# Performance work log

Measured on AMD Instinct MI355X. Metric: run time of the kernel, lower is better.

The kernel has to match this reference:

```python
import jax, jax.numpy as jnp
import numpy as np

T, N, D, H = 512, 64, 1024, 1024  # time, batch(envs), input dim, hidden dim


def setup_inputs() -> dict:
    key = jax.random.key(0)
    ks = jax.random.split(key, 7)
    x = jax.random.normal(ks[0], (T, N, D), jnp.float32)
    hx = jax.random.normal(ks[1], (N, H), jnp.float32)
    mask = (jax.random.uniform(ks[2], (T, N)) > 0.05).astype(jnp.float32)
    s = float(1.0 / np.sqrt(H))
    w_ih = jax.random.uniform(ks[3], (3 * H, D), jnp.float32, -s, s)
    w_hh = jax.random.uniform(ks[4], (3 * H, H), jnp.float32, -s, s)
    b_ih = jax.random.uniform(ks[5], (3 * H,), jnp.float32, -s, s)
    b_hh = jax.random.uniform(ks[6], (3 * H,), jnp.float32, -s, s)
    return {"x": x, "hx": hx, "mask": mask, "w_ih": w_ih, "w_hh": w_hh,
            "b_ih": b_ih, "b_hh": b_hh}


def reference(x, hx, mask, w_ih, w_hh, b_ih, b_hh):
    """Masked GRU scan, equivalent to the segment-splitting torch loop:
    h is multiplied by mask[t] before every step (mask==1 inside episodes,
    0 at episode boundaries, so this matches masking only at segment starts).
    """
    # Precompute input projections for all timesteps in one big GEMM: [T,N,3H]
    gi = jnp.einsum('tnd,gd->tng', x, w_ih) + b_ih

    def step(h, inp):
        gi_t, m_t = inp                       # [N,3H], [N]
        h = h * m_t[:, None]                  # reset hidden at episode starts
        gh = h @ w_hh.T + b_hh                # [N,3H]
        i_r, i_z, i_n = jnp.split(gi_t, 3, axis=-1)
        h_r, h_z, h_n = jnp.split(gh, 3, axis=-1)
        r = jax.nn.sigmoid(i_r + h_r)
        z = jax.nn.sigmoid(i_z + h_z)
        n = jnp.tanh(i_n + r * h_n)
        h_new = (1.0 - z) * n + z * h
        return h_new, h_new

    h_final, out = jax.lax.scan(step, hx, (gi, mask))
    return out, h_final
```

## Files before the change

### kernel.cpp

```cpp
#include <hip/hip_runtime.h>

#define TT 512
#define NN 64
#define DD 1024
#define HH 1024

typedef __attribute__((ext_vector_type(8))) short bf16x8;
typedef __attribute__((ext_vector_type(4))) float f32x4;
typedef __attribute__((ext_vector_type(8))) unsigned short u16x8;
typedef __attribute__((ext_vector_type(4))) int i32x4;

__device__ unsigned short g_wih[192u * 2048 * 8];
__device__ unsigned short g_whh[192u * 2048 * 8];
__device__ unsigned short g_x[2048u * 2048 * 8];
__device__ unsigned short g_gi[(size_t)2048 * 64 * 768];
__device__ unsigned g_hbuf32[2u * 4 * 16384];

__device__ __forceinline__ unsigned short f2bf(float f) {
  unsigned u = __float_as_uint(f);
  u += 0x7fffu + ((u >> 16) & 1u);
  return (unsigned short)(u >> 16);
}

__global__ void prep_kernel(const float* __restrict__ x,
                            const float* __restrict__ wih,
                            const float* __restrict__ whh) {
  const int gsz = gridDim.x * blockDim.x;
  const int gid = blockIdx.x * blockDim.x + threadIdx.x;
  for (int z = gid; z < 2 * 4 * 16384; z += gsz) g_hbuf32[z] = 0u;

  const int W8 = 192 * 2048;
  const int X8 = 2048 * 2048;
  for (int idx = gid; idx < 2 * W8 + X8; idx += gsz) {
    if (idx < 2 * W8) {
      const float* src = (idx < W8) ? wih : whh;
      unsigned short* dst = (idx < W8) ? g_wih : g_whh;
      int i8 = (idx < W8) ? idx : idx - W8;
      size_t g = (size_t)i8 * 8;
      int col = (int)(g >> 10);
      int k = (int)(g & 1023);
      int kk = k >> 5, lg = (k >> 3) & 3;
      int cg = col >> 4;
      int l = (col & 15) | (lg << 4);
      size_t o8 = ((size_t)cg * 32 + kk) * 64 + l;
      const float* p = src + g;
      float4 v0 = *(const float4*)(p);
      float4 v1 = *(const float4*)(p + 4);
      u16x8 u;
      u[0] = f2bf(v0.x); u[1] = f2bf(v0.y); u[2] = f2bf(v0.z); u[3] = f2bf(v0.w);
      u[4] = f2bf(v1.x); u[5] = f2bf(v1.y); u[6] = f2bf(v1.z); u[7] = f2bf(v1.w);
      *(u16x8*)(dst + o8 * 8) = u;
    } else {
      int i8 = idx - 2 * W8;
      size_t g = (size_t)i8 * 8;
      int row = (int)(g >> 10);
      int k = (int)(g & 1023);
      int t = row >> 6, env = row & 63;
      int eg = env >> 4;
      int kk = k >> 5, lg = (k >> 3) & 3;
      int l = (env & 15) | (lg << 4);
      size_t o8 = (((size_t)t * 4 + eg) * 32 + kk) * 64 + l;
      const float* p = x + g;
      float4 v0 = *(const float4*)(p);
      float4 v1 = *(const float4*)(p + 4);
      u16x8 u;
      u[0] = f2bf(v0.x); u[1] = f2bf(v0.y); u[2] = f2bf(v0.z); u[3] = f2bf(v0.w);
      u[4] = f2bf(v1.x); u[5] = f2bf(v1.y); u[6] = f2bf(v1.z); u[7] = f2bf(v1.w);
      *(u16x8*)(g_x + o8 * 8) = u;
    }
  }
}

__global__ __launch_bounds__(256) void gemm_gi() {
  extern __shared__ char smem[];
  unsigned short* As = (unsigned short*)smem;
  unsigned short* Bs = As + 2048 * 8;
  const int tid = threadIdx.x;
  const int bid = blockIdx.x;
  const int mblk = bid & 255, nblk = bid >> 8;
  const int w = tid >> 6, l = tid & 63;
  const int wm = w >> 1, wn = w & 1;

  u16x8 pa[8], pb[8];
  #pragma unroll
  for (int i = 0; i < 8; ++i) {
    int e = tid + i * 256;
    int mt = e >> 8, kkl = (e >> 6) & 3, lane = e & 63;
    pa[i] = *((const u16x8*)g_x  + ((size_t)(mblk * 8 + mt) * 32 + kkl) * 64 + lane);
    pb[i] = *((const u16x8*)g_wih + ((size_t)(nblk * 8 + mt) * 32 + kkl) * 64 + lane);
  }
  f32x4 acc[4][4] = {};
  for (int c = 0; c < 8; ++c) {
    __syncthreads();
    #pragma unroll
    for (int i = 0; i < 8; ++i) {
      int e = tid + i * 256;
      ((u16x8*)As)[e] = pa[i];
      ((u16x8*)Bs)[e] = pb[i];
    }
    __syncthreads();
    if (c < 7) {
      #pragma unroll
      for (int i = 0; i < 8; ++i) {
        int e = tid + i * 256;
        int mt = e >> 8, kkl = (e >> 6) & 3, lane = e & 63;
        pa[i] = *((const u16x8*)g_x  + ((size_t)(mblk * 8 + mt) * 32 + (c + 1) * 4 + kkl) * 64 + lane);
        pb[i] = *((const u16x8*)g_wih + ((size_t)(nblk * 8 + mt) * 32 + (c + 1) * 4 + kkl) * 64 + lane);
      }
    }
    #pragma unroll
    for (int kkl = 0; kkl < 4; ++kkl) {
      bf16x8 af[4], bfr[4];
      #pragma unroll
      for (int ai = 0; ai < 4; ++ai) af[ai]  = ((const bf16x8*)As)[((wm * 4 + ai) * 4 + kkl) * 64 + l];
      #pragma unroll
      for (int bi = 0; bi < 4; ++bi) bfr[bi] = ((const bf16x8*)Bs)[((wn * 4 + bi) * 4 + kkl) * 64 + l];
      #pragma unroll
      for (int ai = 0; ai < 4; ++ai)
        #pragma unroll
        for (int bi = 0; bi < 4; ++bi)
          acc[ai][bi] = __builtin_amdgcn_mfma_f32_16x16x32_bf16(af[ai], bfr[bi], acc[ai][bi], 0, 0, 0);
    }
  }
  const int jj = l & 15;
  #pragma unroll
  for (int ai = 0; ai < 4; ++ai)
    #pragma unroll
    for (int bi = 0; bi < 4; ++bi) {
      int mt = mblk * 8 + wm * 4 + ai;
      int nt = nblk * 8 + wn * 4 + bi;
      int gate = nt >> 6, jg = nt & 63;
      size_t base = ((size_t)mt * 64 + jg) * 768 + (size_t)gate * 256;
      #pragma unroll
      for (int i = 0; i < 4; ++i) {
        int env = (l >> 4) * 4 + i;
        g_gi[base + env * 16 + jj] = f2bf(acc[ai][bi][i]);
      }
    }
}

__global__ __launch_bounds__(256) void scan_kernel(const float* __restrict__ hx,
                                                   const float* __restrict__ mask,
                                                   const float* __restrict__ bih,
                                                   const float* __restrict__ bhh,
                                                   float* __restrict__ out) {
  extern __shared__ char smem[];
  unsigned short* whhL = (unsigned short*)smem;
  unsigned short* hA   = whhL + 3 * 2048 * 8;
  float* Cl = (float*)(hA + 2048 * 8);

  const int tid = threadIdx.x;
  const int bid = blockIdx.x;
  const int eg = bid >> 6, jg = bid & 63;
  const int e0 = eg * 16;
  const int w3 = tid >> 6, l = tid & 63;
  const int e_ = tid >> 4, jj = tid & 15;
  const int j = jg * 16 + jj;

  #pragma unroll 4
  for (int i = 0; i < 24; ++i) {
    int e = tid + i * 256;
    int gate = e >> 11, rem = e & 2047;
    ((u16x8*)whhL)[e] = *((const u16x8*)g_whh + (size_t)(gate * 64 + jg) * 2048 + rem);
  }

  const int kf = jg * 16 + jj;
  const int widx = (((kf >> 5) * 64) + (e_ | (((kf >> 3) & 3) << 4))) * 8 + (kf & 7);

  float hreg;
  {
    float h0 = hx[(size_t)(e0 + e_) * HH + j] * mask[e0 + e_];
    hreg = h0;
    unsigned tw = (1u << 16) | (unsigned)f2bf(h0);
    unsigned* dst = g_hbuf32 + ((size_t)eg << 14) + widx;
    asm volatile("global_store_dword %0, %1, off sc0 sc1" :: "v"(dst), "v"(tw) : "memory");
  }

  const float br  = bih[j] + bhh[j];
  const float bz  = bih[HH + j] + bhh[HH + j];
  const float bin = bih[2 * HH + j];
  const float bhn = bhh[2 * HH + j];

  unsigned short pgr, pgz, pgn;
  {
    size_t gb = ((size_t)eg * 64 + jg) * 768;
    pgr = g_gi[gb + tid]; pgz = g_gi[gb + 256 + tid]; pgn = g_gi[gb + 512 + tid];
  }

  const unsigned voff = (unsigned)tid * 32;

  for (int t = 0; t < TT; ++t) {
    int tm = (t + 1 < TT) ? (t + 1) : (TT - 1);
    float mnext = mask[tm * NN + e0 + e_];

    const unsigned* hb = g_hbuf32 + (((size_t)(t & 1) * 4 + eg) << 14);
    const unsigned tagp = (unsigned)(t + 1) << 16;
    i32x4 hv[16];
    while (true) {
      #pragma unroll
      for (int i = 0; i < 8; ++i) {
        asm volatile("global_load_dwordx4 %0, %2, %3 sc0 sc1\n\t"
                     "global_load_dwordx4 %1, %2, %3 offset:16 sc0 sc1"
                     : "=&v"(hv[2 * i]), "=&v"(hv[2 * i + 1])
                     : "v"(voff), "s"(hb + i * 2048));
      }
      asm volatile("s_waitcnt vmcnt(0)" ::: "memory");
      __builtin_amdgcn_sched_barrier(0);
      unsigned bad = 0;
      #pragma unroll
      for (int i = 0; i < 16; ++i) {
        bad |= ((unsigned)hv[i][0] ^ tagp); bad |= ((unsigned)hv[i][1] ^ tagp);
        bad |= ((unsigned)hv[i][2] ^ tagp); bad |= ((unsigned)hv[i][3] ^ tagp);
      }
      bad &= 0xFFFF0000u;
      if (__all(bad == 0)) break;
      __builtin_amdgcn_s_sleep(1);
    }

    #pragma unroll
    for (int i = 0; i < 8; ++i) {
      i32x4 a = hv[2 * i], b = hv[2 * i + 1];
      i32x4 pk;
      pk[0] = (int)__builtin_amdgcn_perm((unsigned)a[1], (unsigned)a[0], 0x05040100u);
      pk[1] = (int)__builtin_amdgcn_perm((unsigned)a[3], (unsigned)a[2], 0x05040100u);
      pk[2] = (int)__builtin_amdgcn_perm((unsigned)b[1], (unsigned)b[0], 0x05040100u);
      pk[3] = (int)__builtin_amdgcn_perm((unsigned)b[3], (unsigned)b[2], 0x05040100u);
      ((i32x4*)hA)[tid + i * 256] = pk;
    }
    __syncthreads();

    float gr  = __uint_as_float((unsigned)pgr << 16);
    float gz  = __uint_as_float((unsigned)pgz << 16);
    float gn_ = __uint_as_float((unsigned)pgn << 16);
    if (t + 1 < TT) {
      size_t gb = ((size_t)((t + 1) * 4 + eg) * 64 + jg) * 768;
      pgr = g_gi[gb + tid]; pgz = g_gi[gb + 256 + tid]; pgn = g_gi[gb + 512 + tid];
    }

    if (w3 < 3) {
      const bf16x8* ap = (const bf16x8*)hA;
      const bf16x8* bp = (const bf16x8*)whhL + (size_t)w3 * 2048;
      f32x4 acc0 = {0.f, 0.f, 0.f, 0.f}, acc1 = {0.f, 0.f, 0.f, 0.f};
      #pragma unroll 8
      for (int kk = 0; kk < 16; ++kk) {
        acc0 = __builtin_amdgcn_mfma_f32_16x16x32_bf16(ap[kk * 64 + l], bp[kk * 64 + l], acc0, 0, 0, 0);
        acc1 = __builtin_amdgcn_mfma_f32_16x16x32_bf16(ap[(kk + 16) * 64 + l], bp[(kk + 16) * 64 + l], acc1, 0, 0, 0);
      }
      int col = l & 15, r0 = (l >> 4) * 4;
      #pragma unroll
      for (int i = 0; i < 4; ++i) Cl[w3 * 256 + (r0 + i) * 16 + col] = acc0[i] + acc1[i];
    }
    __syncthreads();

    {
      float pr = gr + Cl[tid] + br;
      float pz = gz + Cl[256 + tid] + bz;
      float r = 1.f / (1.f + __expf(-pr));
      float z = 1.f / (1.f + __expf(-pz));
      float hn = Cl[512 + tid] + bhn;
      float gn = gn_ + bin + r * hn;
      float e2g = __expf(2.f * gn);
      float n = 1.f - 2.f / (e2g + 1.f);
      float hnew = (1.f - z) * n + z * hreg;
      if (t + 1 < TT) {
        float hm = hnew * mnext;
        hreg = hm;
        unsigned tw = ((unsigned)(t + 2) << 16) | (unsigned)f2bf(hm);
        unsigned* dst = g_hbuf32 + (((size_t)((t + 1) & 1) * 4 + eg) << 14) + widx;
        asm volatile("global_store_dword %0, %1, off sc0 sc1" :: "v"(dst), "v"(tw) : "memory");
      }
      out[(size_t)t * NN * HH + (size_t)(e0 + e_) * HH + j] = hnew;
      if (t == TT - 1)
        out[(size_t)TT * NN * HH + (size_t)(e0 + e_) * HH + j] = hnew;
    }
  }
}

extern "C" void kernel_launch(void* const* d_in, const int* in_sizes, int n_in,
                              void* d_out, int out_size, void* d_ws, size_t ws_size,
                              hipStream_t stream) {
  (void)in_sizes; (void)n_in; (void)d_ws; (void)ws_size; (void)out_size;
  const float* x    = (const float*)d_in[0];
  const float* hx   = (const float*)d_in[1];
  const float* mask = (const float*)d_in[2];
  const float* wih  = (const float*)d_in[3];
  const float* whh  = (const float*)d_in[4];
  const float* bih  = (const float*)d_in[5];
  const float* bhh  = (const float*)d_in[6];
  float* out = (float*)d_out;

  hipFuncSetAttribute((const void*)gemm_gi, hipFuncAttributeMaxDynamicSharedMemorySize, 65536);
  hipFuncSetAttribute((const void*)scan_kernel, hipFuncAttributeMaxDynamicSharedMemorySize, 134144);

  prep_kernel<<<2048, 256, 0, stream>>>(x, wih, whh);
  gemm_gi<<<6144, 256, 65536, stream>>>();
  scan_kernel<<<256, 256, 134144, stream>>>(hx, mask, bih, bhh, out);
}
```

Before: 2.304 ms.

## Replace tagged-value polling with per-block flags and bf16 hidden buffer

Drops the scheme where every hidden value carries a 16-bit timestep tag that all waves poll. Hidden state is now stored as plain bf16, and each producer block publishes one flag after a store drain and a block barrier. Consumers spin on 64 flags, then read half as many bytes without any repacking. The MFMA reduction is also split across four independent accumulators to shorten the dependency chain. The cost is an extra vmcnt wait plus a __syncthreads before each flag store, and ordering correctness now relies on sc0/sc1 visibility between the data and the flag.

```diff
diff --git a/kernel.cpp b/kernel.cpp
--- a/kernel.cpp
+++ b/kernel.cpp
@@ -14,7 +14,8 @@
 __device__ unsigned short g_whh[192u * 2048 * 8];
 __device__ unsigned short g_x[2048u * 2048 * 8];
 __device__ unsigned short g_gi[(size_t)2048 * 64 * 768];
-__device__ unsigned g_hbuf32[2u * 4 * 16384];
+__device__ unsigned short g_hbuf[2u * 4 * 16384];
+__device__ int g_flags[256];
 
 __device__ __forceinline__ unsigned short f2bf(float f) {
   unsigned u = __float_as_uint(f);
@@ -27,7 +28,7 @@
                             const float* __restrict__ whh) {
   const int gsz = gridDim.x * blockDim.x;
   const int gid = blockIdx.x * blockDim.x + threadIdx.x;
-  for (int z = gid; z < 2 * 4 * 16384; z += gsz) g_hbuf32[z] = 0u;
+  if (gid < 256) g_flags[gid] = 0;
 
   const int W8 = 192 * 2048;
   const int X8 = 2048 * 2048;
@@ -171,9 +172,16 @@
   {
     float h0 = hx[(size_t)(e0 + e_) * HH + j] * mask[e0 + e_];
     hreg = h0;
-    unsigned tw = (1u << 16) | (unsigned)f2bf(h0);
-    unsigned* dst = g_hbuf32 + ((size_t)eg << 14) + widx;
-    asm volatile("global_store_dword %0, %1, off sc0 sc1" :: "v"(dst), "v"(tw) : "memory");
+    unsigned short* dst = g_hbuf + ((size_t)eg << 14) + widx;
+    unsigned hw = (unsigned)f2bf(h0);
+    asm volatile("global_store_short %0, %1, off sc0 sc1" :: "v"(dst), "v"(hw) : "memory");
+  }
+  asm volatile("s_waitcnt vmcnt(0)" ::: "memory");
+  __syncthreads();
+  if (tid == 0) {
+    int* fdst = g_flags + eg * 64 + jg;
+    int one = 1;
+    asm volatile("global_store_dword %0, %1, off sc0 sc1" :: "v"(fdst), "v"(one) : "memory");
   }
 
   const float br  = bih[j] + bhh[j];
@@ -187,46 +195,34 @@
     pgr = g_gi[gb + tid]; pgz = g_gi[gb + 256 + tid]; pgn = g_gi[gb + 512 + tid];
   }
 
-  const unsigned voff = (unsigned)tid * 32;
+  const unsigned voff = (unsigned)tid * 16;
+  const int* fp = g_flags + eg * 64 + l;
 
   for (int t = 0; t < TT; ++t) {
     int tm = (t + 1 < TT) ? (t + 1) : (TT - 1);
     float mnext = mask[tm * NN + e0 + e_];
 
-    const unsigned* hb = g_hbuf32 + (((size_t)(t & 1) * 4 + eg) << 14);
-    const unsigned tagp = (unsigned)(t + 1) << 16;
-    i32x4 hv[16];
+    const int target = t + 1;
     while (true) {
-      #pragma unroll
-      for (int i = 0; i < 8; ++i) {
-        asm volatile("global_load_dwordx4 %0, %2, %3 sc0 sc1\n\t"
-                     "global_load_dwordx4 %1, %2, %3 offset:16 sc0 sc1"
-                     : "=&v"(hv[2 * i]), "=&v"(hv[2 * i + 1])
-                     : "v"(voff), "s"(hb + i * 2048));
-      }
-      asm volatile("s_waitcnt vmcnt(0)" ::: "memory");
-      __builtin_amdgcn_sched_barrier(0);
-      unsigned bad = 0;
-      #pragma unroll
-      for (int i = 0; i < 16; ++i) {
-        bad |= ((unsigned)hv[i][0] ^ tagp); bad |= ((unsigned)hv[i][1] ^ tagp);
-        bad |= ((unsigned)hv[i][2] ^ tagp); bad |= ((unsigned)hv[i][3] ^ tagp);
-      }
-      bad &= 0xFFFF0000u;
-      if (__all(bad == 0)) break;
-      __builtin_amdgcn_s_sleep(1);
-    }
-
+      int v;
+      asm volatile("global_load_dword %0, %1, off sc0 sc1\n\t"
+                   "s_waitcnt vmcnt(0)"
+                   : "=v"(v) : "v"(fp) : "memory");
+      if (__all(v >= target)) break;
+    }
+    __builtin_amdgcn_sched_barrier(0);
+
+    const unsigned* hb = (const unsigned*)g_hbuf + (((size_t)(t & 1) * 4 + eg) << 13);
+    i32x4 hv[8];
     #pragma unroll
     for (int i = 0; i < 8; ++i) {
-      i32x4 a = hv[2 * i], b = hv[2 * i + 1];
-      i32x4 pk;
-      pk[0] = (int)__builtin_amdgcn_perm((unsigned)a[1], (unsigned)a[0], 0x05040100u);
-      pk[1] = (int)__builtin_amdgcn_perm((unsigned)a[3], (unsigned)a[2], 0x05040100u);
-      pk[2] = (int)__builtin_amdgcn_perm((unsigned)b[1], (unsigned)b[0], 0x05040100u);
-      pk[3] = (int)__builtin_amdgcn_perm((unsigned)b[3], (unsigned)b[2], 0x05040100u);
-      ((i32x4*)hA)[tid + i * 256] = pk;
-    }
+      asm volatile("global_load_dwordx4 %0, %1, %2 sc0 sc1"
+                   : "=v"(hv[i]) : "v"(voff), "s"(hb + i * 1024));
+    }
+    asm volatile("s_waitcnt vmcnt(0)" ::: "memory");
+    __builtin_amdgcn_sched_barrier(0);
+    #pragma unroll
+    for (int i = 0; i < 8; ++i) ((i32x4*)hA)[tid + i * 256] = hv[i];
     __syncthreads();
 
     float gr  = __uint_as_float((unsigned)pgr << 16);
@@ -240,15 +236,21 @@
     if (w3 < 3) {
       const bf16x8* ap = (const bf16x8*)hA;
       const bf16x8* bp = (const bf16x8*)whhL + (size_t)w3 * 2048;
-      f32x4 acc0 = {0.f, 0.f, 0.f, 0.f}, acc1 = {0.f, 0.f, 0.f, 0.f};
+      f32x4 a0 = {0.f,0.f,0.f,0.f}, a1 = {0.f,0.f,0.f,0.f};
+      f32x4 a2 = {0.f,0.f,0.f,0.f}, a3 = {0.f,0.f,0.f,0.f};
       #pragma unroll 8
-      for (int kk = 0; kk < 16; ++kk) {
-        acc0 = __builtin_amdgcn_mfma_f32_16x16x32_bf16(ap[kk * 64 + l], bp[kk * 64 + l], acc0, 0, 0, 0);
-        acc1 = __builtin_amdgcn_mfma_f32_16x16x32_bf16(ap[(kk + 16) * 64 + l], bp[(kk + 16) * 64 + l], acc1, 0, 0, 0);
+      for (int kk = 0; kk < 8; ++kk) {
+        a0 = __builtin_amdgcn_mfma_f32_16x16x32_bf16(ap[kk * 64 + l],        bp[kk * 64 + l],        a0, 0, 0, 0);
+        a1 = __builtin_amdgcn_mfma_f32_16x16x32_bf16(ap[(kk + 8) * 64 + l],  bp[(kk + 8) * 64 + l],  a1, 0, 0, 0);
+        a2 = __builtin_amdgcn_mfma_f32_16x16x32_bf16(ap[(kk + 16) * 64 + l], bp[(kk + 16) * 64 + l], a2, 0, 0, 0);
+        a3 = __builtin_amdgcn_mfma_f32_16x16x32_bf16(ap[(kk + 24) * 64 + l], bp[(kk + 24) * 64 + l], a3, 0, 0, 0);
       }
+      f32x4 s01, s23, s;
+      #pragma unroll
+      for (int i = 0; i < 4; ++i) { s01[i] = a0[i] + a1[i]; s23[i] = a2[i] + a3[i]; s[i] = s01[i] + s23[i]; }
       int col = l & 15, r0 = (l >> 4) * 4;
       #pragma unroll
-      for (int i = 0; i < 4; ++i) Cl[w3 * 256 + (r0 + i) * 16 + col] = acc0[i] + acc1[i];
+      for (int i = 0; i < 4; ++i) Cl[w3 * 256 + (r0 + i) * 16 + col] = s[i];
     }
     __syncthreads();
 
@@ -262,13 +264,22 @@
       float e2g = __expf(2.f * gn);
       float n = 1.f - 2.f / (e2g + 1.f);
       float hnew = (1.f - z) * n + z * hreg;
+
       if (t + 1 < TT) {
         float hm = hnew * mnext;
         hreg = hm;
-        unsigned tw = ((unsigned)(t + 2) << 16) | (unsigned)f2bf(hm);
-        unsigned* dst = g_hbuf32 + (((size_t)((t + 1) & 1) * 4 + eg) << 14) + widx;
-        asm volatile("global_store_dword %0, %1, off sc0 sc1" :: "v"(dst), "v"(tw) : "memory");
+        unsigned short* dst = g_hbuf + (((size_t)((t + 1) & 1) * 4 + eg) << 14) + widx;
+        unsigned hw = (unsigned)f2bf(hm);
+        asm volatile("global_store_short %0, %1, off sc0 sc1" :: "v"(dst), "v"(hw) : "memory");
+        asm volatile("s_waitcnt vmcnt(0)" ::: "memory");
+        __syncthreads();
+        if (tid == 0) {
+          int* fdst = g_flags + eg * 64 + jg;
+          int fv = t + 2;
+          asm volatile("global_store_dword %0, %1, off sc0 sc1" :: "v"(fdst), "v"(fv) : "memory");
+        }
       }
+
       out[(size_t)t * NN * HH + (size_t)(e0 + e_) * HH + j] = hnew;
       if (t == TT - 1)
         out[(size_t)TT * NN * HH + (size_t)(e0 + e_) * HH + j] = hnew;
```

Measured after the change: 2.886 ms. +25.2%, slower.

## Poll hidden-state exchange per chunk with 64-slot ring and remapped blocks

Applied to the files above, without the earlier changes.

Enlarges the tagged hidden-state exchange buffer from a double buffer to a 64-slot ring and remaps block ids so blocks sharing an env group are spread differently. The first read now uses plain loads, and only the stale chunks are re-polled with coherent loads, with ready chunks packed into LDS as they arrive. The h@W_hh MFMA loop is split into four independent accumulators, and the mask load is moved after the poll. The aim is to cut cross-block spin latency and MFMA dependency stalls. The risk is that the first non-coherent read may see cached stale data, forcing a retry pass, and the larger buffer costs more zero-initialisation in prep.

```diff
diff --git a/kernel.cpp b/kernel.cpp
--- a/kernel.cpp
+++ b/kernel.cpp
@@ -9,12 +9,13 @@
 typedef __attribute__((ext_vector_type(4))) float f32x4;
 typedef __attribute__((ext_vector_type(8))) unsigned short u16x8;
 typedef __attribute__((ext_vector_type(4))) int i32x4;
+typedef __attribute__((ext_vector_type(2))) int i32x2;
 
 __device__ unsigned short g_wih[192u * 2048 * 8];
 __device__ unsigned short g_whh[192u * 2048 * 8];
 __device__ unsigned short g_x[2048u * 2048 * 8];
 __device__ unsigned short g_gi[(size_t)2048 * 64 * 768];
-__device__ unsigned g_hbuf32[2u * 4 * 16384];
+__device__ unsigned g_hbuf32[64u * 4 * 16384];
 
 __device__ __forceinline__ unsigned short f2bf(float f) {
   unsigned u = __float_as_uint(f);
@@ -27,7 +28,7 @@
                             const float* __restrict__ whh) {
   const int gsz = gridDim.x * blockDim.x;
   const int gid = blockIdx.x * blockDim.x + threadIdx.x;
-  for (int z = gid; z < 2 * 4 * 16384; z += gsz) g_hbuf32[z] = 0u;
+  for (int z = gid; z < 64 * 4 * 16384; z += gsz) g_hbuf32[z] = 0u;
 
   const int W8 = 192 * 2048;
   const int X8 = 2048 * 2048;
@@ -151,7 +152,8 @@
 
   const int tid = threadIdx.x;
   const int bid = blockIdx.x;
-  const int eg = bid >> 6, jg = bid & 63;
+  const int eg = (bid & 7) >> 1;
+  const int jg = ((bid >> 3) << 1) | (bid & 1);
   const int e0 = eg * 16;
   const int w3 = tid >> 6, l = tid & 63;
   const int e_ = tid >> 4, jj = tid & 15;
@@ -187,45 +189,48 @@
     pgr = g_gi[gb + tid]; pgz = g_gi[gb + 256 + tid]; pgn = g_gi[gb + 512 + tid];
   }
 
-  const unsigned voff = (unsigned)tid * 32;
+  const unsigned voff = (unsigned)tid * 16;
 
   for (int t = 0; t < TT; ++t) {
-    int tm = (t + 1 < TT) ? (t + 1) : (TT - 1);
-    float mnext = mask[tm * NN + e0 + e_];
-
-    const unsigned* hb = g_hbuf32 + (((size_t)(t & 1) * 4 + eg) << 14);
+    const unsigned* hb = g_hbuf32 + ((((size_t)(t & 63)) * 4 + eg) << 14);
     const unsigned tagp = (unsigned)(t + 1) << 16;
+    const i32x4* hp = (const i32x4*)hb + tid;
     i32x4 hv[16];
-    while (true) {
-      #pragma unroll
-      for (int i = 0; i < 8; ++i) {
-        asm volatile("global_load_dwordx4 %0, %2, %3 sc0 sc1\n\t"
-                     "global_load_dwordx4 %1, %2, %3 offset:16 sc0 sc1"
-                     : "=&v"(hv[2 * i]), "=&v"(hv[2 * i + 1])
-                     : "v"(voff), "s"(hb + i * 2048));
+    #pragma unroll
+    for (int c = 0; c < 16; ++c) hv[c] = hp[c * 256];
+
+    unsigned stale = 0;
+    #pragma unroll
+    for (int c = 0; c < 16; ++c) {
+      unsigned bad = (((unsigned)hv[c][0] ^ tagp) | ((unsigned)hv[c][1] ^ tagp) |
+                      ((unsigned)hv[c][2] ^ tagp) | ((unsigned)hv[c][3] ^ tagp)) & 0xFFFF0000u;
+      if (bad) stale |= (1u << c);
+      else {
+        i32x2 pk;
+        pk[0] = (int)__builtin_amdgcn_perm((unsigned)hv[c][1], (unsigned)hv[c][0], 0x05040100u);
+        pk[1] = (int)__builtin_amdgcn_perm((unsigned)hv[c][3], (unsigned)hv[c][2], 0x05040100u);
+        ((i32x2*)hA)[c * 256 + tid] = pk;
+      }
+    }
+    while (__any(stale != 0)) {
+      #pragma unroll
+      for (int c = 0; c < 16; ++c) if (stale & (1u << c)) {
+        asm volatile("global_load_dwordx4 %0, %1, %2 sc0 sc1"
+                     : "=v"(hv[c]) : "v"(voff), "s"((const void*)(hb + c * 1024)));
       }
       asm volatile("s_waitcnt vmcnt(0)" ::: "memory");
-      __builtin_amdgcn_sched_barrier(0);
-      unsigned bad = 0;
-      #pragma unroll
-      for (int i = 0; i < 16; ++i) {
-        bad |= ((unsigned)hv[i][0] ^ tagp); bad |= ((unsigned)hv[i][1] ^ tagp);
-        bad |= ((unsigned)hv[i][2] ^ tagp); bad |= ((unsigned)hv[i][3] ^ tagp);
-      }
-      bad &= 0xFFFF0000u;
-      if (__all(bad == 0)) break;
-      __builtin_amdgcn_s_sleep(1);
-    }
-
-    #pragma unroll
-    for (int i = 0; i < 8; ++i) {
-      i32x4 a = hv[2 * i], b = hv[2 * i + 1];
-      i32x4 pk;
-      pk[0] = (int)__builtin_amdgcn_perm((unsigned)a[1], (unsigned)a[0], 0x05040100u);
-      pk[1] = (int)__builtin_amdgcn_perm((unsigned)a[3], (unsigned)a[2], 0x05040100u);
-      pk[2] = (int)__builtin_amdgcn_perm((unsigned)b[1], (unsigned)b[0], 0x05040100u);
-      pk[3] = (int)__builtin_amdgcn_perm((unsigned)b[3], (unsigned)b[2], 0x05040100u);
-      ((i32x4*)hA)[tid + i * 256] = pk;
+      #pragma unroll
+      for (int c = 0; c < 16; ++c) if (stale & (1u << c)) {
+        unsigned bad = (((unsigned)hv[c][0] ^ tagp) | ((unsigned)hv[c][1] ^ tagp) |
+                        ((unsigned)hv[c][2] ^ tagp) | ((unsigned)hv[c][3] ^ tagp)) & 0xFFFF0000u;
+        if (!bad) {
+          i32x2 pk;
+          pk[0] = (int)__builtin_amdgcn_perm((unsigned)hv[c][1], (unsigned)hv[c][0], 0x05040100u);
+          pk[1] = (int)__builtin_amdgcn_perm((unsigned)hv[c][3], (unsigned)hv[c][2], 0x05040100u);
+          ((i32x2*)hA)[c * 256 + tid] = pk;
+          stale &= ~(1u << c);
+        }
+      }
     }
     __syncthreads();
 
@@ -236,19 +241,27 @@
       size_t gb = ((size_t)((t + 1) * 4 + eg) * 64 + jg) * 768;
       pgr = g_gi[gb + tid]; pgz = g_gi[gb + 256 + tid]; pgn = g_gi[gb + 512 + tid];
     }
+    int tm = (t + 1 < TT) ? (t + 1) : (TT - 1);
+    float mnext = mask[tm * NN + e0 + e_];
 
     if (w3 < 3) {
       const bf16x8* ap = (const bf16x8*)hA;
       const bf16x8* bp = (const bf16x8*)whhL + (size_t)w3 * 2048;
-      f32x4 acc0 = {0.f, 0.f, 0.f, 0.f}, acc1 = {0.f, 0.f, 0.f, 0.f};
+      f32x4 a0 = {0.f,0.f,0.f,0.f}, a1 = {0.f,0.f,0.f,0.f};
+      f32x4 a2 = {0.f,0.f,0.f,0.f}, a3 = {0.f,0.f,0.f,0.f};
       #pragma unroll 8
-      for (int kk = 0; kk < 16; ++kk) {
-        acc0 = __builtin_amdgcn_mfma_f32_16x16x32_bf16(ap[kk * 64 + l], bp[kk * 64 + l], acc0, 0, 0, 0);
-        acc1 = __builtin_amdgcn_mfma_f32_16x16x32_bf16(ap[(kk + 16) * 64 + l], bp[(kk + 16) * 64 + l], acc1, 0, 0, 0);
-      }
+      for (int kk = 0; kk < 8; ++kk) {
+        a0 = __builtin_amdgcn_mfma_f32_16x16x32_bf16(ap[kk * 64 + l],        bp[kk * 64 + l],        a0, 0, 0, 0);
+        a1 = __builtin_amdgcn_mfma_f32_16x16x32_bf16(ap[(kk + 8) * 64 + l],  bp[(kk + 8) * 64 + l],  a1, 0, 0, 0);
+        a2 = __builtin_amdgcn_mfma_f32_16x16x32_bf16(ap[(kk + 16) * 64 + l], bp[(kk + 16) * 64 + l], a2, 0, 0, 0);
+        a3 = __builtin_amdgcn_mfma_f32_16x16x32_bf16(ap[(kk + 24) * 64 + l], bp[(kk + 24) * 64 + l], a3, 0, 0, 0);
+      }
+      f32x4 s;
+      #pragma unroll
+      for (int i = 0; i < 4; ++i) s[i] = (a0[i] + a1[i]) + (a2[i] + a3[i]);
       int col = l & 15, r0 = (l >> 4) * 4;
       #pragma unroll
-      for (int i = 0; i < 4; ++i) Cl[w3 * 256 + (r0 + i) * 16 + col] = acc0[i] + acc1[i];
+      for (int i = 0; i < 4; ++i) Cl[w3 * 256 + (r0 + i) * 16 + col] = s[i];
     }
     __syncthreads();
 
@@ -262,13 +275,15 @@
       float e2g = __expf(2.f * gn);
       float n = 1.f - 2.f / (e2g + 1.f);
       float hnew = (1.f - z) * n + z * hreg;
+
       if (t + 1 < TT) {
         float hm = hnew * mnext;
         hreg = hm;
         unsigned tw = ((unsigned)(t + 2) << 16) | (unsigned)f2bf(hm);
-        unsigned* dst = g_hbuf32 + (((size_t)((t + 1) & 1) * 4 + eg) << 14) + widx;
+        unsigned* dst = g_hbuf32 + ((((size_t)((t + 1) & 63)) * 4 + eg) << 14) + widx;
         asm volatile("global_store_dword %0, %1, off sc0 sc1" :: "v"(dst), "v"(tw) : "memory");
       }
+
       out[(size_t)t * NN * HH + (size_t)(e0 + e_) * HH + j] = hnew;
       if (t == TT - 1)
         out[(size_t)TT * NN * HH + (size_t)(e0 + e_) * HH + j] = hnew;
```

New measurement: 2.536 ms. 10.1% more time.
